# Optimization experiments

Measured on AMD Instinct MI355X. Metric: run time of the kernel, lower is better.

Reference implementation:

```python
import jax, jax.numpy as jnp
import numpy as np

B, N, D_MODEL, H, DH, D_INNER = 4, 1024, 512, 8, 64, 2048
SQRTD = float(np.sqrt(DH))


def _ln(x, g, b, eps=1e-5):
    mu = jnp.mean(x, axis=-1, keepdims=True)
    var = jnp.var(x, axis=-1, keepdims=True)
    return (x - mu) * jax.lax.rsqrt(var + eps) * g + b


def setup_inputs() -> dict:
    key = jax.random.key(0)
    ks = jax.random.split(key, 8)
    s = 1.0 / np.sqrt(D_MODEL)
    si = 1.0 / np.sqrt(D_INNER)
    return {
        "Z": jax.random.normal(ks[0], (B, N, D_MODEL), jnp.float32),
        "D": jax.random.uniform(ks[1], (B, N, N), jnp.float32),
        "new_mask": jnp.zeros((B, N, N), jnp.float32),
        "mask": jnp.ones((B, N, N), jnp.float32),
        "Wqkv": jax.random.uniform(ks[2], (3 * D_MODEL, D_MODEL), jnp.float32, -s, s),
        "bqkv": jnp.zeros((3 * D_MODEL,), jnp.float32),
        "Wo": jax.random.uniform(ks[3], (D_MODEL, H * DH), jnp.float32, -s, s),
        "g1": jnp.ones((D_MODEL,), jnp.float32),
        "b1": jnp.zeros((D_MODEL,), jnp.float32),
        "g2": jnp.ones((D_MODEL,), jnp.float32),
        "b2": jnp.zeros((D_MODEL,), jnp.float32),
        "Wp1": jax.random.uniform(ks[4], (D_INNER, D_MODEL), jnp.float32, -s, s),
        "bp1": jnp.zeros((D_INNER,), jnp.float32),
        "Wp2": jax.random.uniform(ks[5], (D_MODEL, D_INNER), jnp.float32, -si, si),
        "bp2": jnp.zeros((D_MODEL,), jnp.float32),
        "gamma": jnp.ones((1,), jnp.float32),
    }


def reference(Z, D, new_mask, mask, Wqkv, bqkv, Wo, g1, b1, g2, b2, Wp1, bp1, Wp2, bp2, gamma):
    inp = Z
    Zn = _ln(Z, g1, b1)
    qkv = (Zn @ Wqkv.T + bqkv).reshape(B, N, H, 3 * DH)
    # chunk order in torch: Z2=value, Z3=query, Z4=key
    v = qkv[..., :DH]
    q = qkv[..., DH:2 * DH]
    k = qkv[..., 2 * DH:]
    # scores: [b, h, n, m]
    W = jnp.einsum('bnhd,bmhd->bhnm', q, k) / SQRTD
    W = W + new_mask[:, None] - (gamma * D)[:, None]
    W = jax.nn.softmax(W, axis=3) * mask[:, None]
    attn = jnp.einsum('bhnm,bmhd->bnhd', W, v).reshape(B, N, D_MODEL)
    attn_out = jax.nn.leaky_relu(attn) @ Wo.T
    Z2 = attn_out + inp
    Zn2 = _ln(Z2, g2, b2)
    return jax.nn.relu(Zn2 @ Wp1.T + bp1) @ Wp2.T + bp2 + Z2
```

## Files before the change

kernel.cpp:

```cpp
#include <hip/hip_runtime.h>
#include <hip/hip_bf16.h>
#include <cstddef>
#include <cstdint>

#define Bv 4
#define Nv 1024
#define DM 512
#define Hh 8
#define DHv 64
#define TOKc 4096

typedef __attribute__((ext_vector_type(4))) float f32x4;
typedef __attribute__((ext_vector_type(8))) short s16x8;

__device__ __forceinline__ uint32_t f2bf_bits(float f) {
    uint32_t x = __float_as_uint(f);
    return (x + 0x7FFFu + ((x >> 16) & 1u)) >> 16;
}
__device__ __forceinline__ short f2bf(float f) { return (short)f2bf_bits(f); }
__device__ __forceinline__ float bf2f(short s) {
    return __uint_as_float(((uint32_t)(uint16_t)s) << 16);
}

__device__ __forceinline__ void g2lds16(const void* g, void* l) {
    __builtin_amdgcn_global_load_lds(
        (const __attribute__((address_space(1))) void*)g,
        (__attribute__((address_space(3))) void*)l, 16, 0, 0);
}

__global__ __launch_bounds__(256) void conv_all(
    const float* __restrict__ W0, const float* __restrict__ W1,
    const float* __restrict__ W2, const float* __restrict__ W3,
    short* __restrict__ D0, short* __restrict__ D1,
    short* __restrict__ D2, short* __restrict__ D3)
{
    int bid = blockIdx.x;
    const float* s; short* d; int base;
    if (bid < 768)       { s = W0; d = D0; base = bid * 1024; }
    else if (bid < 1024) { s = W1; d = D1; base = (bid - 768) * 1024; }
    else if (bid < 2048) { s = W2; d = D2; base = (bid - 1024) * 1024; }
    else                 { s = W3; d = D3; base = (bid - 2048) * 1024; }
    int i = base + threadIdx.x * 4;
    float4 v = *(const float4*)&s[i];
    short4 o = { f2bf(v.x), f2bf(v.y), f2bf(v.z), f2bf(v.w) };
    *(short4*)&d[i] = o;
}

__global__ __launch_bounds__(256) void prep_bm2(
    const float* __restrict__ Dm, const float* __restrict__ nm,
    const float* __restrict__ mk, const float* __restrict__ gamma,
    uint32_t* __restrict__ out)
{
    int o = (blockIdx.x * 256 + threadIdx.x) * 4;
    float g = gamma[0];
    size_t row = o >> 10;
    int p = o & 1023;
    int t = p >> 5;
    const float* Dr = Dm + row * 1024 + t * 32;
    const float* Nr = nm + row * 1024 + t * 32;
    const float* Mr = mk + row * 1024 + t * 32;
    uint4 ov;
    uint32_t* po = &ov.x;
#pragma unroll
    for (int q = 0; q < 4; q++) {
        int pp = (p & 31) + q;
        int j = (pp >> 1) & 15, half = pp & 1;
        int key = half * 16 + j;
        float bias = Nr[key] - g * Dr[key];
        po[q] = f2bf_bits(bias) | (f2bf_bits(Mr[key]) << 16);
    }
    *(uint4*)&out[o] = ov;
}

__global__ __launch_bounds__(256) void ln_kernel(
    const float* __restrict__ X, const float* __restrict__ g,
    const float* __restrict__ bb, short* __restrict__ Y)
{
    __shared__ float red[8];
    int row = blockIdx.x, tid = threadIdx.x;
    const float* x = X + (size_t)row * DM;
    float v0 = x[tid], v1 = x[tid + 256];
    float s = v0 + v1, ss = v0 * v0 + v1 * v1;
#pragma unroll
    for (int o = 32; o > 0; o >>= 1) {
        s += __shfl_xor(s, o);
        ss += __shfl_xor(ss, o);
    }
    int lane = tid & 63, wid = tid >> 6;
    if (lane == 0) { red[wid] = s; red[4 + wid] = ss; }
    __syncthreads();
    float S = red[0] + red[1] + red[2] + red[3];
    float SS = red[4] + red[5] + red[6] + red[7];
    float mean = S * (1.f / DM);
    float var = SS * (1.f / DM) - mean * mean;
    float rstd = rsqrtf(var + 1e-5f);
    short* y = Y + (size_t)row * DM;
    y[tid]       = f2bf((v0 - mean) * rstd * g[tid]       + bb[tid]);
    y[tid + 256] = f2bf((v1 - mean) * rstd * g[tid + 256] + bb[tid + 256]);
}

template <int EPI, int BM, int BN>
__global__ __launch_bounds__(256) void gemm_bf16(
    const short* __restrict__ A, const short* __restrict__ Bw,
    const float* __restrict__ bias, const float* __restrict__ resid,
    void* __restrict__ C0, short* __restrict__ C2, short* __restrict__ C3,
    int M, int N, int Ks, int Kst)
{
    constexpr int FI = BM / 32, FJ = BN / 32;
    __shared__ short As0[BM * 32];
    __shared__ short As1[BM * 32];
    __shared__ short Bs0[BN * 32];
    __shared__ short Bs1[BN * 32];
    int tid = threadIdx.x;
    int lane = tid & 63, wave = tid >> 6;
    int bm = blockIdx.y * BM, bn = blockIdx.x * BN;
    int wm = (wave >> 1) * (BM / 2), wn = (wave & 1) * (BN / 2);
    int n_lo = lane & 15, quad = lane >> 4;

    f32x4 acc[FI][FJ] = {};

    int koff = (EPI == 4) ? blockIdx.z * Ks : 0;
    int lrow = lane >> 2, lchunk = (lane & 3) * 8;
    const short* Ag = A + (size_t)(bm + wave * (BM / 4) + lrow) * Kst + koff + lchunk;
    const short* Bg = Bw + (size_t)(bn + wave * (BN / 4) + lrow) * Kst + koff + lchunk;

    for (int k0 = 0; k0 < Ks; k0 += 64) {
        __syncthreads();
#pragma unroll
        for (int r = 0; r < BM / 64; r++) {
            g2lds16(Ag + (size_t)r * 16 * Kst + k0,      &As0[(wave * (BM / 4) + r * 16) * 32]);
            g2lds16(Ag + (size_t)r * 16 * Kst + k0 + 32, &As1[(wave * (BM / 4) + r * 16) * 32]);
        }
#pragma unroll
        for (int r = 0; r < BN / 64; r++) {
            g2lds16(Bg + (size_t)r * 16 * Kst + k0,      &Bs0[(wave * (BN / 4) + r * 16) * 32]);
            g2lds16(Bg + (size_t)r * 16 * Kst + k0 + 32, &Bs1[(wave * (BN / 4) + r * 16) * 32]);
        }
        __syncthreads();
        s16x8 af0[FI], af1[FI], bf0[FJ], bf1[FJ];
#pragma unroll
        for (int i = 0; i < FI; i++) {
            af0[i] = *(const s16x8*)&As0[(wm + i * 16 + n_lo) * 32 + quad * 8];
            af1[i] = *(const s16x8*)&As1[(wm + i * 16 + n_lo) * 32 + quad * 8];
        }
#pragma unroll
        for (int j = 0; j < FJ; j++) {
            bf0[j] = *(const s16x8*)&Bs0[(wn + j * 16 + n_lo) * 32 + quad * 8];
            bf1[j] = *(const s16x8*)&Bs1[(wn + j * 16 + n_lo) * 32 + quad * 8];
        }
#pragma unroll
        for (int i = 0; i < FI; i++)
#pragma unroll
            for (int j = 0; j < FJ; j++)
                acc[i][j] = __builtin_amdgcn_mfma_f32_16x16x32_bf16(
                    af0[i], bf0[j], acc[i][j], 0, 0, 0);
#pragma unroll
        for (int i = 0; i < FI; i++)
#pragma unroll
            for (int j = 0; j < FJ; j++)
                acc[i][j] = __builtin_amdgcn_mfma_f32_16x16x32_bf16(
                    af1[i], bf1[j], acc[i][j], 0, 0, 0);
    }

#pragma unroll
    for (int i = 0; i < FI; i++) {
#pragma unroll
        for (int j = 0; j < FJ; j++) {
            int col = bn + wn + j * 16 + n_lo;
#pragma unroll
            for (int r = 0; r < 4; r++) {
                int m = bm + wm + i * 16 + quad * 4 + r;
                float v = acc[i][j][r];
                if (EPI == 0) {
                    v += bias[col];
                    int hh = col / 192;
                    int rr = col - hh * 192;
                    int part = rr >> 6, dd = rr & 63;
                    int bI = m >> 10, nI = m & 1023;
                    if (part == 0)
                        ((short*)C0)[((size_t)((bI * Hh + hh) * DHv + dd)) * Nv + nI] = f2bf(v);
                    else if (part == 1)
                        C2[((size_t)((bI * Hh + hh) * Nv + nI)) * DHv + dd] = f2bf(v);
                    else
                        C3[((size_t)((bI * Hh + hh) * Nv + nI)) * DHv + dd] = f2bf(v);
                } else if (EPI == 1) {
                    ((float*)C0)[(size_t)m * N + col] = v + resid[(size_t)m * N + col];
                } else if (EPI == 2) {
                    v += bias[col];
                    ((short*)C0)[(size_t)m * N + col] = f2bf(v > 0.f ? v : 0.f);
                } else {
                    ((short*)C0)[(size_t)blockIdx.z * M * N + (size_t)m * N + col] = f2bf(v);
                }
            }
        }
    }
}

__global__ __launch_bounds__(256) void combine_mlp2(
    const short* __restrict__ P, const float* __restrict__ bias,
    const float* __restrict__ resid, float* __restrict__ out)
{
    int i = (blockIdx.x * 256 + threadIdx.x) * 4;
    float4 rz = *(const float4*)&resid[i];
    float4 bz = *(const float4*)&bias[i & 511];
    short4 p0 = *(const short4*)&P[i];
    short4 p1 = *(const short4*)&P[i + 2097152];
    float4 o;
    o.x = bf2f(p0.x) + bf2f(p1.x) + bz.x + rz.x;
    o.y = bf2f(p0.y) + bf2f(p1.y) + bz.y + rz.y;
    o.z = bf2f(p0.z) + bf2f(p1.z) + bz.z + rz.z;
    o.w = bf2f(p0.w) + bf2f(p1.w) + bz.w + rz.w;
    *(float4*)&out[i] = o;
}

__global__ __launch_bounds__(256) void attn_mfma(
    const short* __restrict__ Q, const short* __restrict__ K,
    const short* __restrict__ Vt, const uint32_t* __restrict__ Bm,
    short* __restrict__ attn_l)
{
    __shared__ short Ksh[64 * 64];
    __shared__ short Vsh[64 * 64];
    __shared__ uint32_t Bsh[64 * 64];
    __shared__ short Ph[4][16 * 72];

    int tid = threadIdx.x, lane = tid & 63, wave = tid >> 6;
    int n_lo = lane & 15, quad = lane >> 4;

    int bid = blockIdx.x;
    int x = bid & 7, inner = bid >> 3;
    int bh = x * 4 + (inner & 3);
    int qt = inner >> 2;
    int b = bh >> 3, h = bh & 7;
    int q0 = qt * 64;
    int qw = q0 + wave * 16;

    const short* Qp = Q + ((size_t)((b * Hh + h) * Nv + qw)) * DHv;
    const short* Kp = K + ((size_t)((b * Hh + h) * Nv)) * DHv;
    const short* Vp = Vt + ((size_t)((b * Hh + h) * DHv)) * Nv;
    const uint32_t* Bp = Bm + ((size_t)(b * Nv + q0)) * Nv;

    s16x8 a0 = *(const s16x8*)&Qp[n_lo * DHv + quad * 8];
    s16x8 a1 = *(const s16x8*)&Qp[n_lo * DHv + 32 + quad * 8];

    f32x4 O[4] = {};
    float lacc[4] = {0.f, 0.f, 0.f, 0.f};
    short* Pw = Ph[wave];

    for (int kt = 0; kt < 16; ++kt) {
        int key0 = kt * 64;
        __syncthreads();
#pragma unroll
        for (int s = 0; s < 2; s++) {
            int si = wave * 2 + s;
            g2lds16(Kp + (size_t)(key0 + si * 8 + (lane >> 3)) * DHv + (lane & 7) * 8,
                    &Ksh[si * 8 * 64]);
            g2lds16(Vp + (size_t)(si * 8 + (lane >> 3)) * Nv + key0 + (lane & 7) * 8,
                    &Vsh[si * 8 * 64]);
        }
#pragma unroll
        for (int s = 0; s < 4; s++) {
            int si = wave * 4 + s;
            g2lds16(Bp + (size_t)(si * 4 + (lane >> 4)) * Nv + key0 + (lane & 15) * 4,
                    &Bsh[si * 4 * 64]);
        }
        __syncthreads();

#pragma unroll
        for (int c = 0; c < 2; c++) {
            s16x8 k0a = *(const s16x8*)&Ksh[(c * 32 + n_lo) * 64 + quad * 8];
            s16x8 k0b = *(const s16x8*)&Ksh[(c * 32 + n_lo) * 64 + 32 + quad * 8];
            s16x8 k1a = *(const s16x8*)&Ksh[(c * 32 + 16 + n_lo) * 64 + quad * 8];
            s16x8 k1b = *(const s16x8*)&Ksh[(c * 32 + 16 + n_lo) * 64 + 32 + quad * 8];
            f32x4 z = {0.f, 0.f, 0.f, 0.f};
            f32x4 s0 = __builtin_amdgcn_mfma_f32_16x16x32_bf16(
                a1, k0b, __builtin_amdgcn_mfma_f32_16x16x32_bf16(a0, k0a, z, 0, 0, 0), 0, 0, 0);
            f32x4 s1 = __builtin_amdgcn_mfma_f32_16x16x32_bf16(
                a1, k1b, __builtin_amdgcn_mfma_f32_16x16x32_bf16(a0, k1a, z, 0, 0, 0), 0, 0, 0);
#pragma unroll
            for (int i = 0; i < 4; i++) {
                int row = quad * 4 + i;
                uint2 u = *(const uint2*)&Bsh[(wave * 16 + row) * 64 + c * 32 + n_lo * 2];
                float e0 = __expf(fminf(s0[i] * 0.125f + __uint_as_float(u.x << 16), 60.f));
                float e1 = __expf(fminf(s1[i] * 0.125f + __uint_as_float(u.y << 16), 60.f));
                lacc[i] += e0 + e1;
                Pw[row * 72 + c * 32 + n_lo]      = f2bf(e0 * __uint_as_float(u.x & 0xFFFF0000u));
                Pw[row * 72 + c * 32 + 16 + n_lo] = f2bf(e1 * __uint_as_float(u.y & 0xFFFF0000u));
            }
        }

#pragma unroll
        for (int c = 0; c < 2; c++) {
            s16x8 pa = *(const s16x8*)&Pw[n_lo * 72 + c * 32 + quad * 8];
#pragma unroll
            for (int t = 0; t < 4; t++) {
                s16x8 vb = *(const s16x8*)&Vsh[(t * 16 + n_lo) * 64 + c * 32 + quad * 8];
                O[t] = __builtin_amdgcn_mfma_f32_16x16x32_bf16(pa, vb, O[t], 0, 0, 0);
            }
        }
    }

#pragma unroll
    for (int i = 0; i < 4; i++)
#pragma unroll
        for (int off = 1; off < 16; off <<= 1) lacc[i] += __shfl_xor(lacc[i], off);

    float inv[4];
#pragma unroll
    for (int i = 0; i < 4; i++) inv[i] = 1.f / lacc[i];
#pragma unroll
    for (int t = 0; t < 4; t++)
#pragma unroll
        for (int i = 0; i < 4; i++) {
            float o = O[t][i] * inv[i];
            o = o > 0.f ? o : 0.01f * o;
            attn_l[((size_t)(b * Nv + qw + quad * 4 + i)) * DM + h * DHv + t * 16 + n_lo] = f2bf(o);
        }
}

extern "C" void kernel_launch(void* const* d_in, const int* in_sizes, int n_in,
                              void* d_out, int out_size, void* d_ws, size_t ws_size,
                              hipStream_t stream)
{
    const float* Z     = (const float*)d_in[0];
    const float* D     = (const float*)d_in[1];
    const float* nmsk  = (const float*)d_in[2];
    const float* msk   = (const float*)d_in[3];
    const float* Wqkv  = (const float*)d_in[4];
    const float* bqkv  = (const float*)d_in[5];
    const float* Wo    = (const float*)d_in[6];
    const float* g1    = (const float*)d_in[7];
    const float* b1    = (const float*)d_in[8];
    const float* g2    = (const float*)d_in[9];
    const float* b2    = (const float*)d_in[10];
    const float* Wp1   = (const float*)d_in[11];
    const float* bp1   = (const float*)d_in[12];
    const float* Wp2   = (const float*)d_in[13];
    const float* bp2   = (const float*)d_in[14];
    const float* gamma = (const float*)d_in[15];
    float* out = (float*)d_out;
    char* w = (char*)d_ws;

    const size_t MB = 1048576;
    short*    WqkvB = (short*)(w);
    short*    WoB   = (short*)(w + 1572864);
    short*    Wp1B  = (short*)(w + 2 * MB);
    short*    Wp2B  = (short*)(w + 4 * MB);
    float*    Z2    = (float*)(w + 6 * MB);
    uint32_t* Bm    = (uint32_t*)(w + 14 * MB);
    short*    Zn    = (short*)(w + 30 * MB);
    short*    Qb    = (short*)(w + 34 * MB);
    short*    Kb    = (short*)(w + 38 * MB);
    short*    VtB   = (short*)(w + 42 * MB);
    short*    AtnL  = (short*)(w + 30 * MB);
    short*    Zn2   = (short*)(w + 14 * MB);
    short*    Hb    = (short*)(w + 18 * MB);
    short*    Pp    = (short*)(w + 34 * MB);

    conv_all<<<3072, 256, 0, stream>>>(Wqkv, Wo, Wp1, Wp2, WqkvB, WoB, Wp1B, Wp2B);
    prep_bm2<<<4096, 256, 0, stream>>>(D, nmsk, msk, gamma, Bm);
    ln_kernel<<<TOKc, 256, 0, stream>>>(Z, g1, b1, Zn);
    gemm_bf16<0, 128, 64><<<dim3(24, 32), 256, 0, stream>>>(
        Zn, WqkvB, bqkv, nullptr, VtB, Qb, Kb, TOKc, 1536, 512, 512);
    attn_mfma<<<dim3(512), 256, 0, stream>>>(Qb, Kb, VtB, Bm, AtnL);
    gemm_bf16<1, 64, 64><<<dim3(8, 64), 256, 0, stream>>>(
        AtnL, WoB, nullptr, Z, Z2, nullptr, nullptr, TOKc, 512, 512, 512);
    ln_kernel<<<TOKc, 256, 0, stream>>>(Z2, g2, b2, Zn2);
    gemm_bf16<2, 128, 64><<<dim3(32, 32), 256, 0, stream>>>(
        Zn2, Wp1B, bp1, nullptr, Hb, nullptr, nullptr, TOKc, 2048, 512, 512);
    gemm_bf16<4, 128, 64><<<dim3(8, 32, 2), 256, 0, stream>>>(
        Hb, Wp2B, nullptr, nullptr, Pp, nullptr, nullptr, TOKc, 512, 1024, 2048);
    combine_mlp2<<<2048, 256, 0, stream>>>(Pp, bp2, Z2, out);
}
```

Baseline: 235.2 us.

## Fuse prep kernels, enlarge GEMM tiles, 4-way split-K, 128-query attention blocks

Merges the weight conversion and bias/mask packing kernels into one launch to save a launch. Widens the GEMM tiles from 128x64 to 128x128 and changes the MLP2 split-K from 2 to 4, with the combine kernel now summing four partials. Attention blocks grow to 512 threads and cover 128 queries, so each K/V tile loaded into LDS serves twice as many query rows. The cost is more LDS per block, fewer blocks (lower occupancy), and extra partial-buffer traffic in the combine step. The 4-way partial buffer at offset 34 MB must not overlap other live workspace buffers.

```diff
diff --git a/kernel.cpp b/kernel.cpp
--- a/kernel.cpp
+++ b/kernel.cpp
@@ -28,48 +28,48 @@
         (__attribute__((address_space(3))) void*)l, 16, 0, 0);
 }
 
-__global__ __launch_bounds__(256) void conv_all(
+__global__ __launch_bounds__(256) void prep_conv(
+    const float* __restrict__ Dm, const float* __restrict__ nm,
+    const float* __restrict__ mk, const float* __restrict__ gamma,
+    uint32_t* __restrict__ Bm,
     const float* __restrict__ W0, const float* __restrict__ W1,
     const float* __restrict__ W2, const float* __restrict__ W3,
     short* __restrict__ D0, short* __restrict__ D1,
     short* __restrict__ D2, short* __restrict__ D3)
 {
     int bid = blockIdx.x;
-    const float* s; short* d; int base;
-    if (bid < 768)       { s = W0; d = D0; base = bid * 1024; }
-    else if (bid < 1024) { s = W1; d = D1; base = (bid - 768) * 1024; }
-    else if (bid < 2048) { s = W2; d = D2; base = (bid - 1024) * 1024; }
-    else                 { s = W3; d = D3; base = (bid - 2048) * 1024; }
-    int i = base + threadIdx.x * 4;
-    float4 v = *(const float4*)&s[i];
-    short4 o = { f2bf(v.x), f2bf(v.y), f2bf(v.z), f2bf(v.w) };
-    *(short4*)&d[i] = o;
-}
-
-__global__ __launch_bounds__(256) void prep_bm2(
-    const float* __restrict__ Dm, const float* __restrict__ nm,
-    const float* __restrict__ mk, const float* __restrict__ gamma,
-    uint32_t* __restrict__ out)
-{
-    int o = (blockIdx.x * 256 + threadIdx.x) * 4;
-    float g = gamma[0];
-    size_t row = o >> 10;
-    int p = o & 1023;
-    int t = p >> 5;
-    const float* Dr = Dm + row * 1024 + t * 32;
-    const float* Nr = nm + row * 1024 + t * 32;
-    const float* Mr = mk + row * 1024 + t * 32;
-    uint4 ov;
-    uint32_t* po = &ov.x;
-#pragma unroll
-    for (int q = 0; q < 4; q++) {
-        int pp = (p & 31) + q;
-        int j = (pp >> 1) & 15, half = pp & 1;
-        int key = half * 16 + j;
-        float bias = Nr[key] - g * Dr[key];
-        po[q] = f2bf_bits(bias) | (f2bf_bits(Mr[key]) << 16);
-    }
-    *(uint4*)&out[o] = ov;
+    if (bid < 4096) {
+        int o = (bid * 256 + threadIdx.x) * 4;
+        float g = gamma[0];
+        size_t row = o >> 10;
+        int p = o & 1023;
+        int t = p >> 5;
+        const float* Dr = Dm + row * 1024 + t * 32;
+        const float* Nr = nm + row * 1024 + t * 32;
+        const float* Mr = mk + row * 1024 + t * 32;
+        uint4 ov;
+        uint32_t* po = &ov.x;
+#pragma unroll
+        for (int q = 0; q < 4; q++) {
+            int pp = (p & 31) + q;
+            int j = (pp >> 1) & 15, half = pp & 1;
+            int key = half * 16 + j;
+            float bias = Nr[key] - g * Dr[key];
+            po[q] = f2bf_bits(bias) | (f2bf_bits(Mr[key]) << 16);
+        }
+        *(uint4*)&Bm[o] = ov;
+    } else {
+        int cid = bid - 4096;
+        const float* s; short* d; int base;
+        if (cid < 768)       { s = W0; d = D0; base = cid * 1024; }
+        else if (cid < 1024) { s = W1; d = D1; base = (cid - 768) * 1024; }
+        else if (cid < 2048) { s = W2; d = D2; base = (cid - 1024) * 1024; }
+        else                 { s = W3; d = D3; base = (cid - 2048) * 1024; }
+        int i = base + threadIdx.x * 4;
+        float4 v = *(const float4*)&s[i];
+        short4 o = { f2bf(v.x), f2bf(v.y), f2bf(v.z), f2bf(v.w) };
+        *(short4*)&d[i] = o;
+    }
 }
 
 __global__ __launch_bounds__(256) void ln_kernel(
@@ -205,23 +205,25 @@
     float4 bz = *(const float4*)&bias[i & 511];
     short4 p0 = *(const short4*)&P[i];
     short4 p1 = *(const short4*)&P[i + 2097152];
+    short4 p2 = *(const short4*)&P[i + 2 * 2097152];
+    short4 p3 = *(const short4*)&P[i + 3 * 2097152];
     float4 o;
-    o.x = bf2f(p0.x) + bf2f(p1.x) + bz.x + rz.x;
-    o.y = bf2f(p0.y) + bf2f(p1.y) + bz.y + rz.y;
-    o.z = bf2f(p0.z) + bf2f(p1.z) + bz.z + rz.z;
-    o.w = bf2f(p0.w) + bf2f(p1.w) + bz.w + rz.w;
+    o.x = bf2f(p0.x) + bf2f(p1.x) + bf2f(p2.x) + bf2f(p3.x) + bz.x + rz.x;
+    o.y = bf2f(p0.y) + bf2f(p1.y) + bf2f(p2.y) + bf2f(p3.y) + bz.y + rz.y;
+    o.z = bf2f(p0.z) + bf2f(p1.z) + bf2f(p2.z) + bf2f(p3.z) + bz.z + rz.z;
+    o.w = bf2f(p0.w) + bf2f(p1.w) + bf2f(p2.w) + bf2f(p3.w) + bz.w + rz.w;
     *(float4*)&out[i] = o;
 }
 
-__global__ __launch_bounds__(256) void attn_mfma(
+__global__ __launch_bounds__(512) void attn_mfma(
     const short* __restrict__ Q, const short* __restrict__ K,
     const short* __restrict__ Vt, const uint32_t* __restrict__ Bm,
     short* __restrict__ attn_l)
 {
     __shared__ short Ksh[64 * 64];
     __shared__ short Vsh[64 * 64];
-    __shared__ uint32_t Bsh[64 * 64];
-    __shared__ short Ph[4][16 * 72];
+    __shared__ uint32_t Bsh[128 * 64];
+    __shared__ short Ph[8][16 * 72];
 
     int tid = threadIdx.x, lane = tid & 63, wave = tid >> 6;
     int n_lo = lane & 15, quad = lane >> 4;
@@ -231,7 +233,7 @@
     int bh = x * 4 + (inner & 3);
     int qt = inner >> 2;
     int b = bh >> 3, h = bh & 7;
-    int q0 = qt * 64;
+    int q0 = qt * 128;
     int qw = q0 + wave * 16;
 
     const short* Qp = Q + ((size_t)((b * Hh + h) * Nv + qw)) * DHv;
@@ -249,14 +251,10 @@
     for (int kt = 0; kt < 16; ++kt) {
         int key0 = kt * 64;
         __syncthreads();
-#pragma unroll
-        for (int s = 0; s < 2; s++) {
-            int si = wave * 2 + s;
-            g2lds16(Kp + (size_t)(key0 + si * 8 + (lane >> 3)) * DHv + (lane & 7) * 8,
-                    &Ksh[si * 8 * 64]);
-            g2lds16(Vp + (size_t)(si * 8 + (lane >> 3)) * Nv + key0 + (lane & 7) * 8,
-                    &Vsh[si * 8 * 64]);
-        }
+        g2lds16(Kp + (size_t)(key0 + wave * 8 + (lane >> 3)) * DHv + (lane & 7) * 8,
+                &Ksh[wave * 8 * 64]);
+        g2lds16(Vp + (size_t)(wave * 8 + (lane >> 3)) * Nv + key0 + (lane & 7) * 8,
+                &Vsh[wave * 8 * 64]);
 #pragma unroll
         for (int s = 0; s < 4; s++) {
             int si = wave * 4 + s;
@@ -356,18 +354,18 @@
     short*    Hb    = (short*)(w + 18 * MB);
     short*    Pp    = (short*)(w + 34 * MB);
 
-    conv_all<<<3072, 256, 0, stream>>>(Wqkv, Wo, Wp1, Wp2, WqkvB, WoB, Wp1B, Wp2B);
-    prep_bm2<<<4096, 256, 0, stream>>>(D, nmsk, msk, gamma, Bm);
+    prep_conv<<<7168, 256, 0, stream>>>(D, nmsk, msk, gamma, Bm,
+                                        Wqkv, Wo, Wp1, Wp2, WqkvB, WoB, Wp1B, Wp2B);
     ln_kernel<<<TOKc, 256, 0, stream>>>(Z, g1, b1, Zn);
-    gemm_bf16<0, 128, 64><<<dim3(24, 32), 256, 0, stream>>>(
+    gemm_bf16<0, 128, 128><<<dim3(12, 32), 256, 0, stream>>>(
         Zn, WqkvB, bqkv, nullptr, VtB, Qb, Kb, TOKc, 1536, 512, 512);
-    attn_mfma<<<dim3(512), 256, 0, stream>>>(Qb, Kb, VtB, Bm, AtnL);
+    attn_mfma<<<dim3(256), 512, 0, stream>>>(Qb, Kb, VtB, Bm, AtnL);
     gemm_bf16<1, 64, 64><<<dim3(8, 64), 256, 0, stream>>>(
         AtnL, WoB, nullptr, Z, Z2, nullptr, nullptr, TOKc, 512, 512, 512);
     ln_kernel<<<TOKc, 256, 0, stream>>>(Z2, g2, b2, Zn2);
-    gemm_bf16<2, 128, 64><<<dim3(32, 32), 256, 0, stream>>>(
+    gemm_bf16<2, 128, 128><<<dim3(16, 32), 256, 0, stream>>>(
         Zn2, Wp1B, bp1, nullptr, Hb, nullptr, nullptr, TOKc, 2048, 512, 512);
-    gemm_bf16<4, 128, 64><<<dim3(8, 32, 2), 256, 0, stream>>>(
-        Hb, Wp2B, nullptr, nullptr, Pp, nullptr, nullptr, TOKc, 512, 1024, 2048);
+    gemm_bf16<4, 128, 128><<<dim3(4, 32, 4), 256, 0, stream>>>(
+        Hb, Wp2B, nullptr, nullptr, Pp, nullptr, nullptr, TOKc, 512, 512, 2048);
     combine_mlp2<<<2048, 256, 0, stream>>>(Pp, bp2, Z2, out);
 }
```

Measured after the change: 242.6 us. +3.1%, slower.
